# Kernel tuning notes

Hardware: AMD Instinct MI355X
Metric: run time of the kernel (lower is better)

Reference implementation:

```python
import jax, jax.numpy as jnp
import numpy as np

N = 30000   # fluid particles
E = 480000  # edges
F = 4       # fluidFeatures (in channels)
P = 8       # RBF basis size per dim (dims=[8], 1D)
LAYERS = [32, 64, 64, 2]


def hat_basis(x, n):
    # 'linear' RBF: hat functions on n evenly spaced centers in [-1, 1]
    centers = jnp.linspace(-1.0, 1.0, n, dtype=x.dtype)
    spacing = 2.0 / (n - 1)
    return jnp.maximum(0.0, 1.0 - jnp.abs(x[:, None] - centers[None, :]) / spacing)  # [E, n]


def rbf_conv(x, fi, fj, d, W, b, mask, n_nodes):
    # x: [N, Cin]; d: [E, 1] clamped; W: [P, Cin, Cout]; b: [Cout]
    phi = hat_basis(d[:, 0], W.shape[0])      # [E, P]
    xj = x[fj]                                 # gather source features [E, Cin]
    msg = jnp.zeros((xj.shape[0], W.shape[2]), dtype=x.dtype)
    for p in range(W.shape[0]):                # small fixed P=8 loop keeps memory O(E*Cout)
        msg = msg + phi[:, p, None] * (xj @ W[p])
    msg = jnp.where(mask[:, None], msg, 0.0)   # centerIgnore: drop self edges fi==fj
    out = jax.ops.segment_sum(msg, fi, num_segments=n_nodes)  # scatter-reduce to targets
    return out + b


def _xavier(key, shape_in, shape_out):
    lim = float(np.sqrt(6.0 / (shape_in + shape_out)))
    return jax.random.uniform(key, (shape_in, shape_out), jnp.float32, -lim, lim)


def setup_inputs() -> dict:
    key = jax.random.key(0)
    ks = jax.random.split(key, 16)
    fluidFeatures = jax.random.normal(ks[0], (N, F), jnp.float32)
    fi = jax.random.randint(ks[1], (E,), 0, N)
    fj = jax.random.randint(ks[2], (E,), 0, N)
    distances = jax.random.normal(ks[3], (E, 1), jnp.float32)
    # conv channels: 4->32, 64->64, 64->64, 64->2
    cio = [(F, 32), (2 * 32, 64), (64, 64), (64, 2)]
    inp = {"fluidFeatures": fluidFeatures, "fi": fi, "fj": fj, "distances": distances}
    for li, (ci, co) in enumerate(cio):
        inp[f"cW{li}"] = jax.random.normal(ks[4 + li], (P, ci, co), jnp.float32) * (1.0 / np.sqrt(P * ci))
        inp[f"cb{li}"] = jnp.zeros((co,), jnp.float32)
        inp[f"fW{li}"] = _xavier(ks[8 + li], ci, co)   # stored [in, out]
        inp[f"fb{li}"] = jnp.zeros((co,), jnp.float32)
    return inp


def reference(fluidFeatures, fi, fj, distances,
              cW0, cb0, fW0, fb0, cW1, cb1, fW1, fb1,
              cW2, cb2, fW2, fb2, cW3, cb3, fW3, fb3):
    n_nodes = fluidFeatures.shape[0]
    mask = fi != fj                     # centerIgnore (mask instead of filter: jit-safe)
    d = jnp.clip(distances, -1.0, 1.0)

    conv0 = rbf_conv(fluidFeatures, fi, fj, d, cW0, cb0, mask, n_nodes)  # [N, 32]
    lin0 = fluidFeatures @ fW0 + fb0                                      # [N, 32]
    ans = jnp.concatenate([lin0, conv0], axis=1)                          # [N, 64]

    # i = 1: features[0]=32 != features[1]=64 -> no residual
    ansc = jax.nn.relu(ans)
    ans = rbf_conv(ansc, fi, fj, d, cW1, cb1, mask, n_nodes) + (ansc @ fW1 + fb1)
    # i = 2: features[1]==features[2]==64 and shapes match -> residual
    ansc = jax.nn.relu(ans)
    ans = rbf_conv(ansc, fi, fj, d, cW2, cb2, mask, n_nodes) + (ansc @ fW2 + fb2) + ans
    # i = 3: 64 -> 2, no residual
    ansc = jax.nn.relu(ans)
    ans = rbf_conv(ansc, fi, fj, d, cW3, cb3, mask, n_nodes) + (ansc @ fW3 + fb3)

    return ans  # dim == 1 (dims=[8]) -> no /128
```

## Files before the change

kernel.cpp:

```cpp
#include <hip/hip_runtime.h>


#define CAP 48

typedef __attribute__((ext_vector_type(8))) short short8;
typedef __attribute__((ext_vector_type(4))) short short4v;
typedef __attribute__((ext_vector_type(4))) float f32x4;

__device__ __forceinline__ short bf16s(float f) {
  unsigned u = __float_as_uint(f);
  return (short)((u + 0x7FFF + ((u >> 16) & 1)) >> 16);
}
__device__ __forceinline__ float b2f(unsigned short s) {
  return __uint_as_float(((unsigned)s) << 16);
}
__device__ __forceinline__ unsigned pack2(float a, float b) {
  return (unsigned)(unsigned short)bf16s(a) | ((unsigned)(unsigned short)bf16s(b) << 16);
}

__global__ void fill_prep(const float* __restrict__ dist,
                          const int* __restrict__ fi, const int* __restrict__ fj,
                          int* __restrict__ cnt, int* __restrict__ jw, int nE,
                          const float* __restrict__ cW1, const float* __restrict__ fW1,
                          const float* __restrict__ cW2, const float* __restrict__ fW2,
                          short* __restrict__ wt1, short* __restrict__ wt2,
                          const float* __restrict__ X,
                          const float* __restrict__ cW0,
                          const float* __restrict__ fW0,
                          unsigned short* __restrict__ U0, int n,
                          int fillBlocks, int prepBlocks) {
  if ((int)blockIdx.x < fillBlocks) {
    int e = blockIdx.x * blockDim.x + threadIdx.x;
    if (e >= nE) return;
    int i = fi[e], j = fj[e];
    if (i == j) return;
    float d = fminf(1.0f, fmaxf(-1.0f, dist[e]));
    float u = (d + 1.0f) * 3.5f;
    int p = min((int)u, 6);
    float w0 = 1.0f - (u - (float)p);
    int wq = (int)(w0 * 16383.0f + 0.5f);
    int pos = atomicAdd(&cnt[i], 1);
    if (pos < CAP)
      jw[(size_t)i * CAP + pos] = j | (p << 15) | (wq << 18);
  } else if ((int)blockIdx.x < fillBlocks + prepBlocks) {
    int idx = ((int)blockIdx.x - fillBlocks) * blockDim.x + threadIdx.x;
    if (idx >= 2 * 576 * 64) return;
    int sel = idx / (576 * 64);
    int r = idx - sel * (576 * 64);
    int col = r >> 6, ch = r & 63;
    const float* cW = sel ? cW2 : cW1;
    const float* fW = sel ? fW2 : fW1;
    float v;
    if (col < 512) {
      int p = col >> 6, co = col & 63;
      v = cW[((size_t)p * 64 + ch) * 64 + co];
    } else {
      v = fW[(size_t)ch * 64 + (col - 512)];
    }
    (sel ? wt2 : wt1)[(size_t)col * 64 + ch] = bf16s(v);
  } else {
    int idx = ((int)blockIdx.x - fillBlocks - prepBlocks) * blockDim.x + threadIdx.x;
    if (idx >= n * 72) return;
    int i = idx / 72, g = idx - i * 72;
    float4 x = *(const float4*)(X + (size_t)i * 4);
    float xk[4] = {x.x, x.y, x.z, x.w};
    float s[4] = {0, 0, 0, 0};
    if (g < 64) {
      int p = g >> 3;
      int co = (g * 4) & 31;
      #pragma unroll
      for (int k = 0; k < 4; ++k) {
        const float* wr = cW0 + ((size_t)p * 4 + k) * 32 + co;
        #pragma unroll
        for (int c = 0; c < 4; ++c) s[c] = fmaf(xk[k], wr[c], s[c]);
      }
    } else {
      int co = (g - 64) * 4;
      #pragma unroll
      for (int k = 0; k < 4; ++k) {
        const float* wr = fW0 + (size_t)k * 32 + co;
        #pragma unroll
        for (int c = 0; c < 4; ++c) s[c] = fmaf(xk[k], wr[c], s[c]);
      }
    }
    uint2 pk = make_uint2(pack2(s[0], s[1]), pack2(s[2], s[3]));
    *(uint2*)(U0 + (size_t)i * 288 + g * 4) = pk;
  }
}

__global__ __launch_bounds__(1024) void layer0_gemm(
    const unsigned short* __restrict__ U0,
    const int* __restrict__ cnt, const int* __restrict__ jw,
    const float* __restrict__ cb0, const float* __restrict__ fb0,
    const short* __restrict__ WTul,
    unsigned short* __restrict__ UL, int n) {
  __shared__ __align__(16) unsigned short sXa[16 * 64];
  __shared__ __align__(16) short sUL[16 * 584];
  const int tid = threadIdx.x;
  const int w = tid >> 6;
  const int lane = tid & 63;
  const int grp = lane >> 5;
  const int gl = lane & 31;
  const int nodeBase = blockIdx.x * 16;
  const int i = nodeBase + w;
  const bool valid = (i < n);
  const int ic = valid ? i : 0;

  int rec = jw[(size_t)ic * CAP + (lane < CAP ? lane : 0)];
  const int m = valid ? min(cnt[ic], CAP) : 0;
  const int mc = m - 1;
  float accLo = 0.0f, accHi = 0.0f;
  for (int q0 = 0; q0 < m; q0 += 16) {
    unsigned raw[8];
    float ws[8];
    #pragma unroll
    for (int k = 0; k < 8; ++k) {
      int eA = q0 + 2 * k;
      int vA = __builtin_amdgcn_readlane(rec, min(eA, mc));
      int vB = __builtin_amdgcn_readlane(rec, min(eA + 1, mc));
      int v = grp ? vB : vA;
      int j = v & 0x7FFF;
      int p = (v >> 15) & 7;
      float w0 = (float)((unsigned)v >> 18) * (1.0f / 16383.0f);
      float wgt = (gl < 16) ? w0 : (1.0f - w0);
      ws[k] = (eA + grp < m) ? wgt : 0.0f;
      raw[k] = ((const unsigned*)(U0 + (size_t)j * 288 + p * 32))[gl];
    }
    #pragma unroll
    for (int k = 0; k < 8; ++k) {
      accLo = fmaf(ws[k], __uint_as_float(raw[k] << 16), accLo);
      accHi = fmaf(ws[k], __uint_as_float(raw[k] & 0xFFFF0000u), accHi);
    }
  }
  accLo += __shfl_xor(accLo, 16, 64);
  accHi += __shfl_xor(accHi, 16, 64);
  accLo += __shfl_xor(accLo, 32, 64);
  accHi += __shfl_xor(accHi, 32, 64);
  if (lane < 16) {
    const int l = lane;
    float c0v = fmaxf(accLo + cb0[2 * l], 0.0f);
    float c1v = fmaxf(accHi + cb0[2 * l + 1], 0.0f);
    unsigned lr = ((const unsigned*)(U0 + (size_t)ic * 288 + 256))[l];
    float l0 = fmaxf(__uint_as_float(lr << 16) + fb0[2 * l], 0.0f);
    float l1 = fmaxf(__uint_as_float(lr & 0xFFFF0000u) + fb0[2 * l + 1], 0.0f);
    unsigned* row = (unsigned*)(sXa + w * 64);
    row[l] = pack2(l0, l1);
    row[16 + l] = pack2(c0v, c1v);
  }
  __syncthreads();

  const int mrow = lane & 15;
  const int quad = lane >> 4;
  short8 b0 = *(const short8*)(sXa + mrow * 64 + quad * 8);
  short8 b1 = *(const short8*)(sXa + mrow * 64 + quad * 8 + 32);
  for (int t = w; t < 36; t += 16) {
    const short* aBase = WTul + (size_t)(t * 16 + mrow) * 64 + quad * 8;
    short8 a0 = *(const short8*)(aBase);
    short8 a1 = *(const short8*)(aBase + 32);
    f32x4 acc = {0, 0, 0, 0};
    acc = __builtin_amdgcn_mfma_f32_16x16x32_bf16(a0, b0, acc, 0, 0, 0);
    acc = __builtin_amdgcn_mfma_f32_16x16x32_bf16(a1, b1, acc, 0, 0, 0);
    short4v pk;
    #pragma unroll
    for (int reg = 0; reg < 4; ++reg) pk[reg] = bf16s(acc[reg]);
    *(short4v*)(sUL + mrow * 584 + t * 16 + quad * 4) = pk;
  }
  __syncthreads();
  const int r = tid >> 6;
  const int c0 = tid & 63;
  if (nodeBase + r < n) {
    unsigned short* dst = UL + (size_t)(nodeBase + r) * 576;
    #pragma unroll
    for (int chunk = c0; chunk < 72; chunk += 64)
      *(short8*)(dst + chunk * 8) = *(const short8*)(sUL + r * 584 + chunk * 8);
  }
}

__global__ __launch_bounds__(1024) void conv_gemm(
    const unsigned short* __restrict__ ULA,
    const int* __restrict__ cnt, const int* __restrict__ jw,
    const float* __restrict__ cb, const float* __restrict__ fb,
    const short* __restrict__ WTul2,
    float* __restrict__ outAns,
    unsigned short* __restrict__ ULB, int n) {
  __shared__ __align__(16) unsigned short sXa[16 * 64];
  __shared__ __align__(16) short sUL[16 * 584];
  const int tid = threadIdx.x;
  const int w = tid >> 6;
  const int lane = tid & 63;
  const int half = lane >> 5;
  const int pl = lane & 31;
  const int nodeBase = blockIdx.x * 16;
  const int i = nodeBase + w;
  const bool valid = (i < n);
  const int ic = valid ? i : 0;

  int rec = jw[(size_t)ic * CAP + (lane < CAP ? lane : 0)];
  const int m = valid ? min(cnt[ic], CAP) : 0;
  const int mc = m - 1;
  const unsigned Lraw = ((const unsigned*)(ULA + (size_t)ic * 576 + 512))[pl];
  float accLo = 0.0f, accHi = 0.0f;
  for (int q0 = 0; q0 < m; q0 += 16) {
    unsigned raw[16];
    float w0s[16];
    #pragma unroll
    for (int k = 0; k < 16; ++k) {
      int v = __builtin_amdgcn_readlane(rec, min(q0 + k, mc));
      int j = v & 0x7FFF;
      int p = (v >> 15) & 7;
      w0s[k] = (float)((unsigned)v >> 18) * (1.0f / 16383.0f);
      raw[k] = ((const unsigned*)(ULA + (size_t)j * 576 + p * 64))[lane];
    }
    #pragma unroll
    for (int k = 0; k < 16; ++k) {
      bool ok = (q0 + k < m);
      float wv = half ? (1.0f - w0s[k]) : w0s[k];
      wv = ok ? wv : 0.0f;
      accLo = fmaf(wv, __uint_as_float(raw[k] << 16), accLo);
      accHi = fmaf(wv, __uint_as_float(raw[k] & 0xFFFF0000u), accHi);
    }
  }
  accLo += __shfl_xor(accLo, 32, 64);
  accHi += __shfl_xor(accHi, 32, 64);
  if (half == 0) {
    unsigned* row = (unsigned*)(sXa + w * 64);
    if (valid) {
      const int c0i = 2 * pl, c1i = c0i + 1;
      float o0 = accLo + __uint_as_float(Lraw << 16) + cb[c0i] + fb[c0i];
      float o1 = accHi + __uint_as_float(Lraw & 0xFFFF0000u) + cb[c1i] + fb[c1i];
      *(float2*)(outAns + (size_t)i * 64 + c0i) = make_float2(o0, o1);
      row[pl] = pack2(fmaxf(o0, 0.0f), fmaxf(o1, 0.0f));
    } else {
      row[pl] = 0u;
    }
  }
  __syncthreads();

  const int mrow = lane & 15;
  const int quad = lane >> 4;
  short8 b0 = *(const short8*)(sXa + mrow * 64 + quad * 8);
  short8 b1 = *(const short8*)(sXa + mrow * 64 + quad * 8 + 32);
  for (int t = w; t < 36; t += 16) {
    const short* aBase = WTul2 + (size_t)(t * 16 + mrow) * 64 + quad * 8;
    short8 a0 = *(const short8*)(aBase);
    short8 a1 = *(const short8*)(aBase + 32);
    f32x4 acc = {0, 0, 0, 0};
    acc = __builtin_amdgcn_mfma_f32_16x16x32_bf16(a0, b0, acc, 0, 0, 0);
    acc = __builtin_amdgcn_mfma_f32_16x16x32_bf16(a1, b1, acc, 0, 0, 0);
    short4v pk;
    #pragma unroll
    for (int reg = 0; reg < 4; ++reg) pk[reg] = bf16s(acc[reg]);
    *(short4v*)(sUL + mrow * 584 + t * 16 + quad * 4) = pk;
  }
  __syncthreads();
  const int r = tid >> 6;
  const int c0 = tid & 63;
  if (nodeBase + r < n) {
    unsigned short* dst = ULB + (size_t)(nodeBase + r) * 576;
    #pragma unroll
    for (int chunk = c0; chunk < 72; chunk += 64)
      *(short8*)(dst + chunk * 8) = *(const short8*)(sUL + r * 584 + chunk * 8);
  }
}

__global__ __launch_bounds__(256) void conv2_kernel(
    const unsigned short* __restrict__ UL,
    const int* __restrict__ cnt, const int* __restrict__ jw,
    const float* __restrict__ cb, const float* __restrict__ fb,
    const float* __restrict__ resid,
    const float* __restrict__ cW3,
    float* __restrict__ T,
    unsigned short* __restrict__ outAnsc, int n) {
  const int lane = threadIdx.x & 63;
  const int half = lane >> 5;
  const int pl = lane & 31;
  const int i = (blockIdx.x * blockDim.x + threadIdx.x) >> 6;
  if (i >= n) return;
  int rec = jw[(size_t)i * CAP + (lane < CAP ? lane : 0)];
  const int m = min(cnt[i], CAP);
  const int mc = m - 1;
  const unsigned Lraw = ((const unsigned*)(UL + (size_t)i * 576 + 512))[pl];
  float2 rv = *(const float2*)(resid + (size_t)i * 64 + 2 * pl);
  float accLo = 0.0f, accHi = 0.0f;
  for (int q0 = 0; q0 < m; q0 += 16) {
    unsigned raw[16];
    float w0s[16];
    #pragma unroll
    for (int k = 0; k < 16; ++k) {
      int v = __builtin_amdgcn_readlane(rec, min(q0 + k, mc));
      int j = v & 0x7FFF;
      int p = (v >> 15) & 7;
      w0s[k] = (float)((unsigned)v >> 18) * (1.0f / 16383.0f);
      raw[k] = ((const unsigned*)(UL + (size_t)j * 576 + p * 64))[lane];
    }
    #pragma unroll
    for (int k = 0; k < 16; ++k) {
      bool ok = (q0 + k < m);
      float wv = half ? (1.0f - w0s[k]) : w0s[k];
      wv = ok ? wv : 0.0f;
      accLo = fmaf(wv, __uint_as_float(raw[k] << 16), accLo);
      accHi = fmaf(wv, __uint_as_float(raw[k] & 0xFFFF0000u), accHi);
    }
  }
  accLo += __shfl_xor(accLo, 32, 64);
  accHi += __shfl_xor(accHi, 32, 64);
  if (half == 0) {
    const int c0i = 2 * pl, c1i = c0i + 1;
    float o0 = accLo + __uint_as_float(Lraw << 16) + cb[c0i] + fb[c0i] + rv.x;
    float o1 = accHi + __uint_as_float(Lraw & 0xFFFF0000u) + cb[c1i] + fb[c1i] + rv.y;
    unsigned short xb0 = (unsigned short)bf16s(fmaxf(o0, 0.0f));
    unsigned short xb1 = (unsigned short)bf16s(fmaxf(o1, 0.0f));
    ((unsigned*)(outAnsc + (size_t)i * 64))[pl] = (unsigned)xb0 | ((unsigned)xb1 << 16);
    float x0 = b2f(xb0), x1 = b2f(xb1);
    float c[16];
    #pragma unroll
    for (int t = 0; t < 16; ++t) {
      const float* wrow = cW3 + ((size_t)(t >> 1) * 64) * 2 + (t & 1);
      c[t] = x0 * wrow[c0i * 2] + x1 * wrow[c1i * 2];
    }
    #pragma unroll
    for (int off = 16; off > 0; off >>= 1) {
      #pragma unroll
      for (int t = 0; t < 16; ++t) c[t] += __shfl_xor(c[t], off, 64);
    }
    if (pl == 0) {
      float* tr = T + (size_t)i * 16;
      #pragma unroll
      for (int t = 0; t < 16; ++t) tr[t] = c[t];
    }
  }
}

__global__ __launch_bounds__(256, 4) void layer3_kernel(
    const unsigned short* __restrict__ Xb,
    const float* __restrict__ T,
    const int* __restrict__ cnt, const int* __restrict__ jw,
    const float* __restrict__ cb3, const float* __restrict__ fb3,
    const float* __restrict__ fW3,
    float* __restrict__ out, int n) {
  const int lane = threadIdx.x & 63;
  const int i = (blockIdx.x * blockDim.x + threadIdx.x) >> 6;
  if (i >= n) return;
  const int m = min(cnt[i], CAP);
  float c0 = 0.0f, c1 = 0.0f;
  if (lane < m) {
    int v = jw[(size_t)i * CAP + lane];
    int j = min(v & 0x7FFF, n - 1);
    int p = (v >> 15) & 7;
    float w0 = (float)((unsigned)v >> 18) * (1.0f / 16383.0f);
    float w1 = 1.0f - w0;
    const float* tb = T + (size_t)j * 16 + p * 2;
    float2 ta = *(const float2*)(tb);
    float2 tc = *(const float2*)(tb + 2);
    c0 = w0 * ta.x + w1 * tc.x;
    c1 = w0 * ta.y + w1 * tc.y;
  }
  float xi = b2f(Xb[(size_t)i * 64 + lane]);
  float2 fw = *(const float2*)(fW3 + lane * 2);
  c0 = fmaf(xi, fw.x, c0);
  c1 = fmaf(xi, fw.y, c1);
  #pragma unroll
  for (int off = 32; off > 0; off >>= 1) {
    c0 += __shfl_xor(c0, off, 64);
    c1 += __shfl_xor(c1, off, 64);
  }
  if (lane == 0) {
    out[(size_t)i * 2 + 0] = c0 + cb3[0] + fb3[0];
    out[(size_t)i * 2 + 1] = c1 + cb3[1] + fb3[1];
  }
}

extern "C" void kernel_launch(void* const* d_in, const int* in_sizes, int n_in,
                              void* d_out, int out_size, void* d_ws, size_t ws_size,
                              hipStream_t stream) {
  const float* X    = (const float*)d_in[0];
  const int*   fi   = (const int*)d_in[1];
  const int*   fj   = (const int*)d_in[2];
  const float* dist = (const float*)d_in[3];
  const float* cW0 = (const float*)d_in[4];  const float* cb0 = (const float*)d_in[5];
  const float* fW0 = (const float*)d_in[6];  const float* fb0 = (const float*)d_in[7];
  const float* cW1 = (const float*)d_in[8];  const float* cb1 = (const float*)d_in[9];
  const float* fW1 = (const float*)d_in[10]; const float* fb1 = (const float*)d_in[11];
  const float* cW2 = (const float*)d_in[12]; const float* cb2 = (const float*)d_in[13];
  const float* fW2 = (const float*)d_in[14]; const float* fb2 = (const float*)d_in[15];
  const float* cW3 = (const float*)d_in[16]; const float* cb3 = (const float*)d_in[17];
  const float* fW3 = (const float*)d_in[18]; const float* fb3 = (const float*)d_in[19];
  float* out = (float*)d_out;

  const int n  = in_sizes[0] / 4;
  const int nE = in_sizes[1];

  unsigned short* ULA   = (unsigned short*)d_ws;
  unsigned short* ULB   = ULA + (size_t)n * 576;
  unsigned short* U0    = ULB;
  float*          ans1  = (float*)(ULB + (size_t)n * 576);
  unsigned short* ansc2 = (unsigned short*)(ans1 + (size_t)n * 64);
  float* T     = (float*)(ansc2 + (size_t)n * 64);
  short* wtul1 = (short*)(T + (size_t)n * 16);
  short* wtul2 = wtul1 + 576 * 64;
  int*   jw    = (int*)(wtul2 + 576 * 64);
  int*   cnt   = jw + (size_t)n * CAP;

  hipMemsetAsync(cnt, 0, (size_t)n * sizeof(int), stream);
  const int fillBlocks = (nE + 255) / 256;
  const int prepBlocks = (2 * 576 * 64 + 255) / 256;
  const int u0Blocks   = (n * 72 + 255) / 256;
  fill_prep<<<fillBlocks + prepBlocks + u0Blocks, 256, 0, stream>>>(
      dist, fi, fj, cnt, jw, nE, cW1, fW1, cW2, fW2, wtul1, wtul2,
      X, cW0, fW0, U0, n, fillBlocks, prepBlocks);

  layer0_gemm<<<(n + 15) / 16, 1024, 0, stream>>>(U0, cnt, jw, cb0, fb0,
                                                  wtul1, ULA, n);
  conv_gemm<<<(n + 15) / 16, 1024, 0, stream>>>(ULA, cnt, jw, cb1, fb1,
                                                wtul2, ans1, ULB, n);
  conv2_kernel<<<(n * 64 + 255) / 256, 256, 0, stream>>>(
      ULB, cnt, jw, cb2, fb2, ans1, cW3, T, ansc2, n);
  layer3_kernel<<<(n * 64 + 255) / 256, 256, 0, stream>>>(ansc2, T, cnt, jw,
                                                          cb3, fb3, fW3, out, n);
}
```

Measured before the change: 251.3 us.

## Issue two gather batches up front and unroll MFMA tail across all tiles

The edge-gather loops in the layer-0, conv, and conv2 kernels now issue the first two 16-edge batches of neighbour loads before any FMA, with sched_barrier separating loads from math, so more loads are in flight per wave. Edge weights are recomputed from the packed record at FMA time rather than held in registers. The MFMA projection tail is factored into a helper that loads all weight tiles for a wave (2 or 3) before issuing MFMAs, and launch bounds add a min-blocks hint of 8. This trades higher register pressure and some redundant readlanes for more memory-level parallelism, with a risk of spills or lower occupancy.

Result: faster. 246.3 us (-2.0%).

```diff
diff --git a/kernel.cpp b/kernel.cpp
--- a/kernel.cpp
+++ b/kernel.cpp
@@ -88,7 +88,51 @@
   }
 }
 
-__global__ __launch_bounds__(1024) void layer0_gemm(
+__device__ __forceinline__ void gemm_tail(const unsigned short* sXa, short* sUL,
+                                          const short* __restrict__ WT,
+                                          int w, int lane) {
+  const int mrow = lane & 15;
+  const int quad = lane >> 4;
+  short8 b0 = *(const short8*)(sXa + mrow * 64 + quad * 8);
+  short8 b1 = *(const short8*)(sXa + mrow * 64 + quad * 8 + 32);
+  const short* A0 = WT + (size_t)(w * 16 + mrow) * 64 + quad * 8;
+  const short* A1 = WT + (size_t)((w + 16) * 16 + mrow) * 64 + quad * 8;
+  short8 a00 = *(const short8*)(A0);
+  short8 a01 = *(const short8*)(A0 + 32);
+  short8 a10 = *(const short8*)(A1);
+  short8 a11 = *(const short8*)(A1 + 32);
+  const bool has3 = (w < 4);
+  short8 a20 = {0, 0, 0, 0, 0, 0, 0, 0};
+  short8 a21 = {0, 0, 0, 0, 0, 0, 0, 0};
+  if (has3) {
+    const short* A2 = WT + (size_t)((w + 32) * 16 + mrow) * 64 + quad * 8;
+    a20 = *(const short8*)(A2);
+    a21 = *(const short8*)(A2 + 32);
+  }
+  __builtin_amdgcn_sched_barrier(0);
+  f32x4 acc0 = {0, 0, 0, 0}, acc1 = {0, 0, 0, 0};
+  acc0 = __builtin_amdgcn_mfma_f32_16x16x32_bf16(a00, b0, acc0, 0, 0, 0);
+  acc0 = __builtin_amdgcn_mfma_f32_16x16x32_bf16(a01, b1, acc0, 0, 0, 0);
+  acc1 = __builtin_amdgcn_mfma_f32_16x16x32_bf16(a10, b0, acc1, 0, 0, 0);
+  acc1 = __builtin_amdgcn_mfma_f32_16x16x32_bf16(a11, b1, acc1, 0, 0, 0);
+  short4v pk;
+  #pragma unroll
+  for (int r = 0; r < 4; ++r) pk[r] = bf16s(acc0[r]);
+  *(short4v*)(sUL + mrow * 584 + w * 16 + quad * 4) = pk;
+  #pragma unroll
+  for (int r = 0; r < 4; ++r) pk[r] = bf16s(acc1[r]);
+  *(short4v*)(sUL + mrow * 584 + (w + 16) * 16 + quad * 4) = pk;
+  if (has3) {
+    f32x4 acc2 = {0, 0, 0, 0};
+    acc2 = __builtin_amdgcn_mfma_f32_16x16x32_bf16(a20, b0, acc2, 0, 0, 0);
+    acc2 = __builtin_amdgcn_mfma_f32_16x16x32_bf16(a21, b1, acc2, 0, 0, 0);
+    #pragma unroll
+    for (int r = 0; r < 4; ++r) pk[r] = bf16s(acc2[r]);
+    *(short4v*)(sUL + mrow * 584 + (w + 32) * 16 + quad * 4) = pk;
+  }
+}
+
+__global__ __launch_bounds__(1024, 8) void layer0_gemm(
     const unsigned short* __restrict__ U0,
     const int* __restrict__ cnt, const int* __restrict__ jw,
     const float* __restrict__ cb0, const float* __restrict__ fb0,
@@ -110,28 +154,45 @@
   const int m = valid ? min(cnt[ic], CAP) : 0;
   const int mc = m - 1;
   float accLo = 0.0f, accHi = 0.0f;
-  for (int q0 = 0; q0 < m; q0 += 16) {
-    unsigned raw[8];
-    float ws[8];
-    #pragma unroll
-    for (int k = 0; k < 8; ++k) {
-      int eA = q0 + 2 * k;
-      int vA = __builtin_amdgcn_readlane(rec, min(eA, mc));
-      int vB = __builtin_amdgcn_readlane(rec, min(eA + 1, mc));
-      int v = grp ? vB : vA;
-      int j = v & 0x7FFF;
-      int p = (v >> 15) & 7;
-      float w0 = (float)((unsigned)v >> 18) * (1.0f / 16383.0f);
-      float wgt = (gl < 16) ? w0 : (1.0f - w0);
-      ws[k] = (eA + grp < m) ? wgt : 0.0f;
-      raw[k] = ((const unsigned*)(U0 + (size_t)j * 288 + p * 32))[gl];
-    }
-    #pragma unroll
-    for (int k = 0; k < 8; ++k) {
-      accLo = fmaf(ws[k], __uint_as_float(raw[k] << 16), accLo);
-      accHi = fmaf(ws[k], __uint_as_float(raw[k] & 0xFFFF0000u), accHi);
-    }
-  }
+  const unsigned* __restrict__ u0W = (const unsigned*)U0;
+  unsigned rA[8], rB[8];
+  float wA[8], wB[8];
+#define L0_LOAD(R, WS, Q0)                                                  \
+  _Pragma("unroll")                                                         \
+  for (int k = 0; k < 8; ++k) {                                             \
+    int eA = (Q0) + 2 * k;                                                  \
+    int vA = __builtin_amdgcn_readlane(rec, min(eA, mc));                   \
+    int vB = __builtin_amdgcn_readlane(rec, min(eA + 1, mc));               \
+    int v = grp ? vB : vA;                                                  \
+    int j = v & 0x7FFF;                                                     \
+    int p = (v >> 15) & 7;                                                  \
+    float w0 = (float)((unsigned)v >> 18) * (1.0f / 16383.0f);              \
+    float wgt = (gl < 16) ? w0 : (1.0f - w0);                               \
+    WS[k] = (eA + grp < m) ? wgt : 0.0f;                                    \
+    R[k] = u0W[(size_t)j * 144 + p * 16 + gl];                              \
+  }
+#define L0_FMA(R, WS)                                                       \
+  _Pragma("unroll")                                                         \
+  for (int k = 0; k < 8; ++k) {                                             \
+    accLo = fmaf(WS[k], __uint_as_float(R[k] << 16), accLo);                \
+    accHi = fmaf(WS[k], __uint_as_float(R[k] & 0xFFFF0000u), accHi);        \
+  }
+  if (m > 0) {
+    L0_LOAD(rA, wA, 0);
+    L0_LOAD(rB, wB, 16);
+    __builtin_amdgcn_sched_barrier(0);
+    L0_FMA(rA, wA);
+    if (m > 16) {
+      L0_FMA(rB, wB);
+      for (int q0 = 32; q0 < m; q0 += 16) {
+        L0_LOAD(rA, wA, q0);
+        __builtin_amdgcn_sched_barrier(0);
+        L0_FMA(rA, wA);
+      }
+    }
+  }
+#undef L0_LOAD
+#undef L0_FMA
   accLo += __shfl_xor(accLo, 16, 64);
   accHi += __shfl_xor(accHi, 16, 64);
   accLo += __shfl_xor(accLo, 32, 64);
@@ -149,22 +210,7 @@
   }
   __syncthreads();
 
-  const int mrow = lane & 15;
-  const int quad = lane >> 4;
-  short8 b0 = *(const short8*)(sXa + mrow * 64 + quad * 8);
-  short8 b1 = *(const short8*)(sXa + mrow * 64 + quad * 8 + 32);
-  for (int t = w; t < 36; t += 16) {
-    const short* aBase = WTul + (size_t)(t * 16 + mrow) * 64 + quad * 8;
-    short8 a0 = *(const short8*)(aBase);
-    short8 a1 = *(const short8*)(aBase + 32);
-    f32x4 acc = {0, 0, 0, 0};
-    acc = __builtin_amdgcn_mfma_f32_16x16x32_bf16(a0, b0, acc, 0, 0, 0);
-    acc = __builtin_amdgcn_mfma_f32_16x16x32_bf16(a1, b1, acc, 0, 0, 0);
-    short4v pk;
-    #pragma unroll
-    for (int reg = 0; reg < 4; ++reg) pk[reg] = bf16s(acc[reg]);
-    *(short4v*)(sUL + mrow * 584 + t * 16 + quad * 4) = pk;
-  }
+  gemm_tail(sXa, sUL, WTul, w, lane);
   __syncthreads();
   const int r = tid >> 6;
   const int c0 = tid & 63;
@@ -176,7 +222,7 @@
   }
 }
 
-__global__ __launch_bounds__(1024) void conv_gemm(
+__global__ __launch_bounds__(1024, 8) void conv_gemm(
     const unsigned short* __restrict__ ULA,
     const int* __restrict__ cnt, const int* __restrict__ jw,
     const float* __restrict__ cb, const float* __restrict__ fb,
@@ -200,26 +246,42 @@
   const int mc = m - 1;
   const unsigned Lraw = ((const unsigned*)(ULA + (size_t)ic * 576 + 512))[pl];
   float accLo = 0.0f, accHi = 0.0f;
-  for (int q0 = 0; q0 < m; q0 += 16) {
-    unsigned raw[16];
-    float w0s[16];
-    #pragma unroll
-    for (int k = 0; k < 16; ++k) {
-      int v = __builtin_amdgcn_readlane(rec, min(q0 + k, mc));
-      int j = v & 0x7FFF;
-      int p = (v >> 15) & 7;
-      w0s[k] = (float)((unsigned)v >> 18) * (1.0f / 16383.0f);
-      raw[k] = ((const unsigned*)(ULA + (size_t)j * 576 + p * 64))[lane];
-    }
-    #pragma unroll
-    for (int k = 0; k < 16; ++k) {
-      bool ok = (q0 + k < m);
-      float wv = half ? (1.0f - w0s[k]) : w0s[k];
-      wv = ok ? wv : 0.0f;
-      accLo = fmaf(wv, __uint_as_float(raw[k] << 16), accLo);
-      accHi = fmaf(wv, __uint_as_float(raw[k] & 0xFFFF0000u), accHi);
-    }
-  }
+  const unsigned* __restrict__ ulaW = (const unsigned*)ULA;
+  unsigned rA[16], rB[16];
+#define C1_LOAD(R, Q0)                                                      \
+  _Pragma("unroll")                                                         \
+  for (int k = 0; k < 16; ++k) {                                            \
+    int v = __builtin_amdgcn_readlane(rec, min((Q0) + k, mc));              \
+    int j = v & 0x7FFF;                                                     \
+    int p = (v >> 15) & 7;                                                  \
+    R[k] = ulaW[(size_t)j * 288 + p * 32 + lane];                           \
+  }
+#define C1_FMA(R, Q0)                                                       \
+  _Pragma("unroll")                                                         \
+  for (int k = 0; k < 16; ++k) {                                            \
+    int v = __builtin_amdgcn_readlane(rec, min((Q0) + k, mc));              \
+    float w0 = (float)((unsigned)v >> 18) * (1.0f / 16383.0f);              \
+    float wv = half ? (1.0f - w0) : w0;                                     \
+    wv = ((Q0) + k < m) ? wv : 0.0f;                                        \
+    accLo = fmaf(wv, __uint_as_float(R[k] << 16), accLo);                   \
+    accHi = fmaf(wv, __uint_as_float(R[k] & 0xFFFF0000u), accHi);           \
+  }
+  if (m > 0) {
+    C1_LOAD(rA, 0);
+    C1_LOAD(rB, 16);
+    __builtin_amdgcn_sched_barrier(0);
+    C1_FMA(rA, 0);
+    if (m > 16) {
+      C1_FMA(rB, 16);
+      for (int q0 = 32; q0 < m; q0 += 16) {
+        C1_LOAD(rA, q0);
+        __builtin_amdgcn_sched_barrier(0);
+        C1_FMA(rA, q0);
+      }
+    }
+  }
+#undef C1_LOAD
+#undef C1_FMA
   accLo += __shfl_xor(accLo, 32, 64);
   accHi += __shfl_xor(accHi, 32, 64);
   if (half == 0) {
@@ -236,22 +298,7 @@
   }
   __syncthreads();
 
-  const int mrow = lane & 15;
-  const int quad = lane >> 4;
-  short8 b0 = *(const short8*)(sXa + mrow * 64 + quad * 8);
-  short8 b1 = *(const short8*)(sXa + mrow * 64 + quad * 8 + 32);
-  for (int t = w; t < 36; t += 16) {
-    const short* aBase = WTul2 + (size_t)(t * 16 + mrow) * 64 + quad * 8;
-    short8 a0 = *(const short8*)(aBase);
-    short8 a1 = *(const short8*)(aBase + 32);
-    f32x4 acc = {0, 0, 0, 0};
-    acc = __builtin_amdgcn_mfma_f32_16x16x32_bf16(a0, b0, acc, 0, 0, 0);
-    acc = __builtin_amdgcn_mfma_f32_16x16x32_bf16(a1, b1, acc, 0, 0, 0);
-    short4v pk;
-    #pragma unroll
-    for (int reg = 0; reg < 4; ++reg) pk[reg] = bf16s(acc[reg]);
-    *(short4v*)(sUL + mrow * 584 + t * 16 + quad * 4) = pk;
-  }
+  gemm_tail(sXa, sUL, WTul2, w, lane);
   __syncthreads();
   const int r = tid >> 6;
   const int c0 = tid & 63;
@@ -263,7 +310,7 @@
   }
 }
 
-__global__ __launch_bounds__(256) void conv2_kernel(
+__global__ __launch_bounds__(256, 8) void conv2_kernel(
     const unsigned short* __restrict__ UL,
     const int* __restrict__ cnt, const int* __restrict__ jw,
     const float* __restrict__ cb, const float* __restrict__ fb,
@@ -282,26 +329,42 @@
   const unsigned Lraw = ((const unsigned*)(UL + (size_t)i * 576 + 512))[pl];
   float2 rv = *(const float2*)(resid + (size_t)i * 64 + 2 * pl);
   float accLo = 0.0f, accHi = 0.0f;
-  for (int q0 = 0; q0 < m; q0 += 16) {
-    unsigned raw[16];
-    float w0s[16];
-    #pragma unroll
-    for (int k = 0; k < 16; ++k) {
-      int v = __builtin_amdgcn_readlane(rec, min(q0 + k, mc));
-      int j = v & 0x7FFF;
-      int p = (v >> 15) & 7;
-      w0s[k] = (float)((unsigned)v >> 18) * (1.0f / 16383.0f);
-      raw[k] = ((const unsigned*)(UL + (size_t)j * 576 + p * 64))[lane];
-    }
-    #pragma unroll
-    for (int k = 0; k < 16; ++k) {
-      bool ok = (q0 + k < m);
-      float wv = half ? (1.0f - w0s[k]) : w0s[k];
-      wv = ok ? wv : 0.0f;
-      accLo = fmaf(wv, __uint_as_float(raw[k] << 16), accLo);
-      accHi = fmaf(wv, __uint_as_float(raw[k] & 0xFFFF0000u), accHi);
-    }
-  }
+  const unsigned* __restrict__ ulW = (const unsigned*)UL;
+  unsigned rA[16], rB[16];
+#define C2_LOAD(R, Q0)                                                      \
+  _Pragma("unroll")                                                         \
+  for (int k = 0; k < 16; ++k) {                                            \
+    int v = __builtin_amdgcn_readlane(rec, min((Q0) + k, mc));              \
+    int j = v & 0x7FFF;                                                     \
+    int p = (v >> 15) & 7;                                                  \
+    R[k] = ulW[(size_t)j * 288 + p * 32 + lane];                            \
+  }
+#define C2_FMA(R, Q0)                                                       \
+  _Pragma("unroll")                                                         \
+  for (int k = 0; k < 16; ++k) {                                            \
+    int v = __builtin_amdgcn_readlane(rec, min((Q0) + k, mc));              \
+    float w0 = (float)((unsigned)v >> 18) * (1.0f / 16383.0f);              \
+    float wv = half ? (1.0f - w0) : w0;                                     \
+    wv = ((Q0) + k < m) ? wv : 0.0f;                                        \
+    accLo = fmaf(wv, __uint_as_float(R[k] << 16), accLo);                   \
+    accHi = fmaf(wv, __uint_as_float(R[k] & 0xFFFF0000u), accHi);           \
+  }
+  if (m > 0) {
+    C2_LOAD(rA, 0);
+    C2_LOAD(rB, 16);
+    __builtin_amdgcn_sched_barrier(0);
+    C2_FMA(rA, 0);
+    if (m > 16) {
+      C2_FMA(rB, 16);
+      for (int q0 = 32; q0 < m; q0 += 16) {
+        C2_LOAD(rA, q0);
+        __builtin_amdgcn_sched_barrier(0);
+        C2_FMA(rA, q0);
+      }
+    }
+  }
+#undef C2_LOAD
+#undef C2_FMA
   accLo += __shfl_xor(accLo, 32, 64);
   accHi += __shfl_xor(accHi, 32, 64);
   if (half == 0) {
```

## Re-encode edge records with precomputed offsets and gather via scalar loads into LDS

Applied to the files above, without the earlier changes.

Edge records now store a precomputed row offset (j*9+p) plus a 12-bit weight and a valid flag. Zeroing the whole record table lets padded slots contribute zero weight without per-edge bounds checks. The aggregation kernels read a node's records with scalar s_load_dwordx4 and gather neighbour rows straight into LDS with global_load_lds, replacing per-lane readlane decoding and register gathers. GEMM blocks shrink from 16 to 8 nodes (512 threads) to raise occupancy, and T rows are padded to 18 floats so the offset encoding indexes it directly. The cost is inline asm with manual waitcnts, lower weight precision, and a larger memset.

Result: slower. 268.0 us (+6.6%).

```diff
diff --git a/kernel.cpp b/kernel.cpp
--- a/kernel.cpp
+++ b/kernel.cpp
@@ -6,6 +6,7 @@
 typedef __attribute__((ext_vector_type(8))) short short8;
 typedef __attribute__((ext_vector_type(4))) short short4v;
 typedef __attribute__((ext_vector_type(4))) float f32x4;
+typedef int v4i __attribute__((ext_vector_type(4)));
 
 __device__ __forceinline__ short bf16s(float f) {
   unsigned u = __float_as_uint(f);
@@ -17,6 +18,61 @@
 __device__ __forceinline__ unsigned pack2(float a, float b) {
   return (unsigned)(unsigned short)bf16s(a) | ((unsigned)(unsigned short)bf16s(b) << 16);
 }
+__device__ __forceinline__ float dec_w0(int v) {
+  return __uint_as_float(0x3F800000u | (((unsigned)v & 0xFFFu) << 11)) - 1.0f;
+}
+__device__ __forceinline__ float dec_sf(int v) {
+  return (float)(((unsigned)v >> 12) & 1u);
+}
+__device__ __forceinline__ unsigned long long rfl64(unsigned long long x) {
+  unsigned lo = __builtin_amdgcn_readfirstlane((unsigned)x);
+  unsigned hi = __builtin_amdgcn_readfirstlane((unsigned)(x >> 32));
+  return ((unsigned long long)hi << 32) | (unsigned long long)lo;
+}
+__device__ __forceinline__ void gload_lds4(const void* g, void* l) {
+  __builtin_amdgcn_global_load_lds(
+      (const __attribute__((address_space(1))) void*)g,
+      (__attribute__((address_space(3))) void*)l, 4, 0, 0);
+}
+
+#define WAIT_VM0 asm volatile("s_waitcnt vmcnt(0)" ::: "memory")
+#define WAIT_LGKM0 asm volatile("s_waitcnt lgkmcnt(0)" ::: "memory")
+
+#define LOAD_RECS32Q(JROW, CPTR, MRAW)                                      \
+  v4i q0, q1, q2, q3, q4, q5, q6, q7;                                       \
+  int MRAW;                                                                 \
+  asm volatile("s_load_dwordx4 %0, %9, 0x0\n\t"                             \
+               "s_load_dwordx4 %1, %9, 0x10\n\t"                            \
+               "s_load_dwordx4 %2, %9, 0x20\n\t"                            \
+               "s_load_dwordx4 %3, %9, 0x30\n\t"                            \
+               "s_load_dwordx4 %4, %9, 0x40\n\t"                            \
+               "s_load_dwordx4 %5, %9, 0x50\n\t"                            \
+               "s_load_dwordx4 %6, %9, 0x60\n\t"                            \
+               "s_load_dwordx4 %7, %9, 0x70\n\t"                            \
+               "s_load_dword %8, %10, 0x0\n\t"                              \
+               "s_waitcnt lgkmcnt(0)"                                       \
+               : "=&s"(q0), "=&s"(q1), "=&s"(q2), "=&s"(q3), "=&s"(q4),     \
+                 "=&s"(q5), "=&s"(q6), "=&s"(q7), "=&s"(MRAW)               \
+               : "s"(JROW), "s"(CPTR)                                       \
+               : "memory")
+
+#define LOAD_RECS16TQ(JROW)                                                 \
+  v4i qt0, qt1, qt2, qt3;                                                   \
+  asm volatile("s_load_dwordx4 %0, %4, 0x80\n\t"                            \
+               "s_load_dwordx4 %1, %4, 0x90\n\t"                            \
+               "s_load_dwordx4 %2, %4, 0xA0\n\t"                            \
+               "s_load_dwordx4 %3, %4, 0xB0\n\t"                            \
+               "s_waitcnt lgkmcnt(0)"                                       \
+               : "=&s"(qt0), "=&s"(qt1), "=&s"(qt2), "=&s"(qt3)             \
+               : "s"(JROW)                                                  \
+               : "memory")
+
+#define RECK(K) ((K) < 4 ? q0[(K) & 3] : (K) < 8 ? q1[(K) & 3] :            \
+                 (K) < 12 ? q2[(K) & 3] : (K) < 16 ? q3[(K) & 3] :          \
+                 (K) < 20 ? q4[(K) & 3] : (K) < 24 ? q5[(K) & 3] :          \
+                 (K) < 28 ? q6[(K) & 3] : q7[(K) & 3])
+#define RECT(K) ((K) < 4 ? qt0[(K) & 3] : (K) < 8 ? qt1[(K) & 3] :          \
+                 (K) < 12 ? qt2[(K) & 3] : qt3[(K) & 3])
 
 __global__ void fill_prep(const float* __restrict__ dist,
                           const int* __restrict__ fi, const int* __restrict__ fj,
@@ -38,10 +94,11 @@
     float u = (d + 1.0f) * 3.5f;
     int p = min((int)u, 6);
     float w0 = 1.0f - (u - (float)p);
-    int wq = (int)(w0 * 16383.0f + 0.5f);
+    int wq = min((int)(w0 * 4096.0f + 0.5f), 4095);
+    unsigned off = (unsigned)(j * 9 + p);
     int pos = atomicAdd(&cnt[i], 1);
     if (pos < CAP)
-      jw[(size_t)i * CAP + pos] = j | (p << 15) | (wq << 18);
+      jw[(size_t)i * CAP + pos] = (int)((off << 13) | 0x1000u | (unsigned)wq);
   } else if ((int)blockIdx.x < fillBlocks + prepBlocks) {
     int idx = ((int)blockIdx.x - fillBlocks) * blockDim.x + threadIdx.x;
     if (idx >= 2 * 576 * 64) return;
@@ -88,50 +145,91 @@
   }
 }
 
-__global__ __launch_bounds__(1024) void layer0_gemm(
+__device__ __forceinline__ void gemm_tail8(const unsigned short* sXa, short* sUL,
+                                           const short* __restrict__ WT,
+                                           int w, int lane) {
+  const int mrow = lane & 15;
+  const int quad = lane >> 4;
+  short8 b0 = *(const short8*)(sXa + mrow * 64 + quad * 8);
+  short8 b1 = *(const short8*)(sXa + mrow * 64 + quad * 8 + 32);
+  for (int t = w; t < 36; t += 8) {
+    const short* A = WT + (size_t)(t * 16 + mrow) * 64 + quad * 8;
+    short8 a0 = *(const short8*)(A);
+    short8 a1 = *(const short8*)(A + 32);
+    f32x4 acc = {0, 0, 0, 0};
+    acc = __builtin_amdgcn_mfma_f32_16x16x32_bf16(a0, b0, acc, 0, 0, 0);
+    acc = __builtin_amdgcn_mfma_f32_16x16x32_bf16(a1, b1, acc, 0, 0, 0);
+    short4v pk;
+    #pragma unroll
+    for (int r = 0; r < 4; ++r) pk[r] = bf16s(acc[r]);
+    *(short4v*)(sUL + mrow * 584 + t * 16 + quad * 4) = pk;
+  }
+}
+
+__global__ __launch_bounds__(512, 8) void layer0_gemm(
     const unsigned short* __restrict__ U0,
     const int* __restrict__ cnt, const int* __restrict__ jw,
     const float* __restrict__ cb0, const float* __restrict__ fb0,
     const short* __restrict__ WTul,
     unsigned short* __restrict__ UL, int n) {
+  __shared__ __align__(16) char smem[8 * 4096];
   __shared__ __align__(16) unsigned short sXa[16 * 64];
-  __shared__ __align__(16) short sUL[16 * 584];
   const int tid = threadIdx.x;
   const int w = tid >> 6;
   const int lane = tid & 63;
   const int grp = lane >> 5;
   const int gl = lane & 31;
-  const int nodeBase = blockIdx.x * 16;
+  const unsigned gl4 = (unsigned)gl * 4u;
+  const int nodeBase = blockIdx.x * 8;
   const int i = nodeBase + w;
   const bool valid = (i < n);
   const int ic = valid ? i : 0;
-
-  int rec = jw[(size_t)ic * CAP + (lane < CAP ? lane : 0)];
-  const int m = valid ? min(cnt[ic], CAP) : 0;
-  const int mc = m - 1;
+  if (tid < 256) ((unsigned*)sXa)[256 + tid] = 0u;
+  const int* jrow = (const int*)rfl64((unsigned long long)(jw + (size_t)ic * CAP));
+  const int* cptr = (const int*)rfl64((unsigned long long)(cnt + ic));
+  LOAD_RECS32Q(jrow, cptr, mraw);
+  const int m = valid ? min(mraw, CAP) : 0;
+  char* ldsW = smem + w * 4096;
+  unsigned* ldsWu = (unsigned*)ldsW;
+  const char* u0B = (const char*)U0;
   float accLo = 0.0f, accHi = 0.0f;
-  for (int q0 = 0; q0 < m; q0 += 16) {
-    unsigned raw[8];
-    float ws[8];
-    #pragma unroll
-    for (int k = 0; k < 8; ++k) {
-      int eA = q0 + 2 * k;
-      int vA = __builtin_amdgcn_readlane(rec, min(eA, mc));
-      int vB = __builtin_amdgcn_readlane(rec, min(eA + 1, mc));
-      int v = grp ? vB : vA;
-      int j = v & 0x7FFF;
-      int p = (v >> 15) & 7;
-      float w0 = (float)((unsigned)v >> 18) * (1.0f / 16383.0f);
-      float wgt = (gl < 16) ? w0 : (1.0f - w0);
-      ws[k] = (eA + grp < m) ? wgt : 0.0f;
-      raw[k] = ((const unsigned*)(U0 + (size_t)j * 288 + p * 32))[gl];
-    }
-    #pragma unroll
-    for (int k = 0; k < 8; ++k) {
-      accLo = fmaf(ws[k], __uint_as_float(raw[k] << 16), accLo);
-      accHi = fmaf(ws[k], __uint_as_float(raw[k] & 0xFFFF0000u), accHi);
-    }
-  }
+#define L0_ISSUE(K, RE)                                                     \
+  { int v_ = grp ? RE(2 * (K) + 1) : RE(2 * (K));                           \
+    unsigned soff_ = (((unsigned)v_) >> 7) & 0xFFFFFFC0u;                   \
+    gload_lds4(u0B + soff_ + gl4, ldsW + (K) * 256); }
+#define L0_CONS(K, RE)                                                      \
+  { int v_ = grp ? RE(2 * (K) + 1) : RE(2 * (K));                           \
+    float w0_ = dec_w0(v_);                                                 \
+    float wgt_ = (gl < 16) ? w0_ : (dec_sf(v_) - w0_);                      \
+    unsigned rd_ = ldsWu[(K) * 64 + lane];                                  \
+    accLo = fmaf(wgt_, __uint_as_float(rd_ << 16), accLo);                  \
+    accHi = fmaf(wgt_, __uint_as_float(rd_ & 0xFFFF0000u), accHi); }
+  if (m > 0) {
+    if (m <= 16) {
+      #pragma unroll
+      for (int k = 0; k < 8; ++k) L0_ISSUE(k, RECK);
+      WAIT_VM0;
+      #pragma unroll
+      for (int k = 0; k < 8; ++k) L0_CONS(k, RECK);
+    } else {
+      #pragma unroll
+      for (int k = 0; k < 16; ++k) L0_ISSUE(k, RECK);
+      WAIT_VM0;
+      #pragma unroll
+      for (int k = 0; k < 16; ++k) L0_CONS(k, RECK);
+      if (m > 32) {
+        LOAD_RECS16TQ(jrow);
+        WAIT_LGKM0;
+        #pragma unroll
+        for (int k = 0; k < 8; ++k) L0_ISSUE(k, RECT);
+        WAIT_VM0;
+        #pragma unroll
+        for (int k = 0; k < 8; ++k) L0_CONS(k, RECT);
+      }
+    }
+  }
+#undef L0_ISSUE
+#undef L0_CONS
   accLo += __shfl_xor(accLo, 16, 64);
   accHi += __shfl_xor(accHi, 16, 64);
   accLo += __shfl_xor(accLo, 32, 64);
@@ -149,77 +247,84 @@
   }
   __syncthreads();
 
-  const int mrow = lane & 15;
-  const int quad = lane >> 4;
-  short8 b0 = *(const short8*)(sXa + mrow * 64 + quad * 8);
-  short8 b1 = *(const short8*)(sXa + mrow * 64 + quad * 8 + 32);
-  for (int t = w; t < 36; t += 16) {
-    const short* aBase = WTul + (size_t)(t * 16 + mrow) * 64 + quad * 8;
-    short8 a0 = *(const short8*)(aBase);
-    short8 a1 = *(const short8*)(aBase + 32);
-    f32x4 acc = {0, 0, 0, 0};
-    acc = __builtin_amdgcn_mfma_f32_16x16x32_bf16(a0, b0, acc, 0, 0, 0);
-    acc = __builtin_amdgcn_mfma_f32_16x16x32_bf16(a1, b1, acc, 0, 0, 0);
-    short4v pk;
-    #pragma unroll
-    for (int reg = 0; reg < 4; ++reg) pk[reg] = bf16s(acc[reg]);
-    *(short4v*)(sUL + mrow * 584 + t * 16 + quad * 4) = pk;
-  }
+  gemm_tail8(sXa, (short*)smem, WTul, w, lane);
   __syncthreads();
-  const int r = tid >> 6;
+  const int r2 = tid >> 6;
   const int c0 = tid & 63;
-  if (nodeBase + r < n) {
-    unsigned short* dst = UL + (size_t)(nodeBase + r) * 576;
+  if (nodeBase + r2 < n) {
+    const short* sUL = (const short*)smem;
+    unsigned short* dst = UL + (size_t)(nodeBase + r2) * 576;
     #pragma unroll
     for (int chunk = c0; chunk < 72; chunk += 64)
-      *(short8*)(dst + chunk * 8) = *(const short8*)(sUL + r * 584 + chunk * 8);
-  }
-}
-
-__global__ __launch_bounds__(1024) void conv_gemm(
+      *(short8*)(dst + chunk * 8) = *(const short8*)(sUL + r2 * 584 + chunk * 8);
+  }
+}
+
+__global__ __launch_bounds__(512, 8) void conv_gemm(
     const unsigned short* __restrict__ ULA,
     const int* __restrict__ cnt, const int* __restrict__ jw,
     const float* __restrict__ cb, const float* __restrict__ fb,
     const short* __restrict__ WTul2,
     float* __restrict__ outAns,
     unsigned short* __restrict__ ULB, int n) {
+  __shared__ __align__(16) char smem[8 * 4096];
   __shared__ __align__(16) unsigned short sXa[16 * 64];
-  __shared__ __align__(16) short sUL[16 * 584];
   const int tid = threadIdx.x;
   const int w = tid >> 6;
   const int lane = tid & 63;
   const int half = lane >> 5;
   const int pl = lane & 31;
-  const int nodeBase = blockIdx.x * 16;
+  const unsigned lane4 = (unsigned)lane * 4u;
+  const int nodeBase = blockIdx.x * 8;
   const int i = nodeBase + w;
   const bool valid = (i < n);
   const int ic = valid ? i : 0;
-
-  int rec = jw[(size_t)ic * CAP + (lane < CAP ? lane : 0)];
-  const int m = valid ? min(cnt[ic], CAP) : 0;
-  const int mc = m - 1;
+  if (tid < 256) ((unsigned*)sXa)[256 + tid] = 0u;
+  const int* jrow = (const int*)rfl64((unsigned long long)(jw + (size_t)ic * CAP));
+  const int* cptr = (const int*)rfl64((unsigned long long)(cnt + ic));
+  LOAD_RECS32Q(jrow, cptr, mraw);
+  const int m = valid ? min(mraw, CAP) : 0;
   const unsigned Lraw = ((const unsigned*)(ULA + (size_t)ic * 576 + 512))[pl];
+  char* ldsW = smem + w * 4096;
+  unsigned* ldsWu = (unsigned*)ldsW;
+  const char* ulB = (const char*)ULA;
   float accLo = 0.0f, accHi = 0.0f;
-  for (int q0 = 0; q0 < m; q0 += 16) {
-    unsigned raw[16];
-    float w0s[16];
-    #pragma unroll
-    for (int k = 0; k < 16; ++k) {
-      int v = __builtin_amdgcn_readlane(rec, min(q0 + k, mc));
-      int j = v & 0x7FFF;
-      int p = (v >> 15) & 7;
-      w0s[k] = (float)((unsigned)v >> 18) * (1.0f / 16383.0f);
-      raw[k] = ((const unsigned*)(ULA + (size_t)j * 576 + p * 64))[lane];
-    }
-    #pragma unroll
-    for (int k = 0; k < 16; ++k) {
-      bool ok = (q0 + k < m);
-      float wv = half ? (1.0f - w0s[k]) : w0s[k];
-      wv = ok ? wv : 0.0f;
-      accLo = fmaf(wv, __uint_as_float(raw[k] << 16), accLo);
-      accHi = fmaf(wv, __uint_as_float(raw[k] & 0xFFFF0000u), accHi);
-    }
-  }
+#define CV_ISSUE(K, RE)                                                     \
+  { unsigned soff_ = (((unsigned)RE(K)) >> 6) & 0xFFFFFF80u;                \
+    gload_lds4(ulB + soff_ + lane4, ldsW + ((K) & 15) * 256); }
+#define CV_CONS(K, RE)                                                      \
+  { int v_ = RE(K);                                                         \
+    float w0_ = dec_w0(v_);                                                 \
+    float wv_ = half ? (dec_sf(v_) - w0_) : w0_;                            \
+    unsigned rd_ = ldsWu[((K) & 15) * 64 + lane];                           \
+    accLo = fmaf(wv_, __uint_as_float(rd_ << 16), accLo);                   \
+    accHi = fmaf(wv_, __uint_as_float(rd_ & 0xFFFF0000u), accHi); }
+  if (m > 0) {
+    #pragma unroll
+    for (int k = 0; k < 16; ++k) CV_ISSUE(k, RECK);
+    WAIT_VM0;
+    #pragma unroll
+    for (int k = 0; k < 16; ++k) CV_CONS(k, RECK);
+    if (m > 16) {
+      WAIT_LGKM0;
+      #pragma unroll
+      for (int k = 16; k < 32; ++k) CV_ISSUE(k, RECK);
+      WAIT_VM0;
+      #pragma unroll
+      for (int k = 16; k < 32; ++k) CV_CONS(k, RECK);
+      if (m > 32) {
+        LOAD_RECS16TQ(jrow);
+        WAIT_LGKM0;
+        #pragma unroll
+        for (int k = 0; k < 16; ++k) CV_ISSUE(k, RECT);
+        WAIT_VM0;
+        #pragma unroll
+        for (int k = 0; k < 16; ++k) CV_CONS(k, RECT);
+      }
+    }
+  }
+#undef CV_ISSUE
+#undef CV_CONS
   accLo += __shfl_xor(accLo, 32, 64);
   accHi += __shfl_xor(accHi, 32, 64);
   if (half == 0) {
@@ -236,34 +341,20 @@
   }
   __syncthreads();
 
-  const int mrow = lane & 15;
-  const int quad = lane >> 4;
-  short8 b0 = *(const short8*)(sXa + mrow * 64 + quad * 8);
-  short8 b1 = *(const short8*)(sXa + mrow * 64 + quad * 8 + 32);
-  for (int t = w; t < 36; t += 16) {
-    const short* aBase = WTul2 + (size_t)(t * 16 + mrow) * 64 + quad * 8;
-    short8 a0 = *(const short8*)(aBase);
-    short8 a1 = *(const short8*)(aBase + 32);
-    f32x4 acc = {0, 0, 0, 0};
-    acc = __builtin_amdgcn_mfma_f32_16x16x32_bf16(a0, b0, acc, 0, 0, 0);
-    acc = __builtin_amdgcn_mfma_f32_16x16x32_bf16(a1, b1, acc, 0, 0, 0);
-    short4v pk;
-    #pragma unroll
-    for (int reg = 0; reg < 4; ++reg) pk[reg] = bf16s(acc[reg]);
-    *(short4v*)(sUL + mrow * 584 + t * 16 + quad * 4) = pk;
-  }
+  gemm_tail8(sXa, (short*)smem, WTul2, w, lane);
   __syncthreads();
-  const int r = tid >> 6;
+  const int r2 = tid >> 6;
   const int c0 = tid & 63;
-  if (nodeBase + r < n) {
-    unsigned short* dst = ULB + (size_t)(nodeBase + r) * 576;
+  if (nodeBase + r2 < n) {
+    const short* sUL = (const short*)smem;
+    unsigned short* dst = ULB + (size_t)(nodeBase + r2) * 576;
     #pragma unroll
     for (int chunk = c0; chunk < 72; chunk += 64)
-      *(short8*)(dst + chunk * 8) = *(const short8*)(sUL + r * 584 + chunk * 8);
-  }
-}
-
-__global__ __launch_bounds__(256) void conv2_kernel(
+      *(short8*)(dst + chunk * 8) = *(const short8*)(sUL + r2 * 584 + chunk * 8);
+  }
+}
+
+__global__ __launch_bounds__(256, 8) void conv2_kernel(
     const unsigned short* __restrict__ UL,
     const int* __restrict__ cnt, const int* __restrict__ jw,
     const float* __restrict__ cb, const float* __restrict__ fb,
@@ -271,37 +362,60 @@
     const float* __restrict__ cW3,
     float* __restrict__ T,
     unsigned short* __restrict__ outAnsc, int n) {
+  __shared__ __align__(16) char smem2[4 * 4096];
   const int lane = threadIdx.x & 63;
   const int half = lane >> 5;
   const int pl = lane & 31;
+  const unsigned lane4 = (unsigned)lane * 4u;
+  const int w4 = threadIdx.x >> 6;
   const int i = (blockIdx.x * blockDim.x + threadIdx.x) >> 6;
   if (i >= n) return;
-  int rec = jw[(size_t)i * CAP + (lane < CAP ? lane : 0)];
-  const int m = min(cnt[i], CAP);
-  const int mc = m - 1;
+  const int* jrow = (const int*)rfl64((unsigned long long)(jw + (size_t)i * CAP));
+  const int* cptr = (const int*)rfl64((unsigned long long)(cnt + i));
+  LOAD_RECS32Q(jrow, cptr, mraw);
+  const int m = min(mraw, CAP);
   const unsigned Lraw = ((const unsigned*)(UL + (size_t)i * 576 + 512))[pl];
   float2 rv = *(const float2*)(resid + (size_t)i * 64 + 2 * pl);
+  char* ldsW = smem2 + w4 * 4096;
+  unsigned* ldsWu = (unsigned*)ldsW;
+  const char* ulB = (const char*)UL;
   float accLo = 0.0f, accHi = 0.0f;
-  for (int q0 = 0; q0 < m; q0 += 16) {
-    unsigned raw[16];
-    float w0s[16];
-    #pragma unroll
-    for (int k = 0; k < 16; ++k) {
-      int v = __builtin_amdgcn_readlane(rec, min(q0 + k, mc));
-      int j = v & 0x7FFF;
-      int p = (v >> 15) & 7;
-      w0s[k] = (float)((unsigned)v >> 18) * (1.0f / 16383.0f);
-      raw[k] = ((const unsigned*)(UL + (size_t)j * 576 + p * 64))[lane];
-    }
-    #pragma unroll
-    for (int k = 0; k < 16; ++k) {
-      bool ok = (q0 + k < m);
-      float wv = half ? (1.0f - w0s[k]) : w0s[k];
-      wv = ok ? wv : 0.0f;
-      accLo = fmaf(wv, __uint_as_float(raw[k] << 16), accLo);
-      accHi = fmaf(wv, __uint_as_float(raw[k] & 0xFFFF0000u), accHi);
-    }
-  }
+#define CV_ISSUE(K, RE)                                                     \
+  { unsigned soff_ = (((unsigned)RE(K)) >> 6) & 0xFFFFFF80u;                \
+    gload_lds4(ulB + soff_ + lane4, ldsW + ((K) & 15) * 256); }
+#define CV_CONS(K, RE)                                                      \
+  { int v_ = RE(K);                                                         \
+    float w0_ = dec_w0(v_);                                                 \
+    float wv_ = half ? (dec_sf(v_) - w0_) : w0_;                            \
+    unsigned rd_ = ldsWu[((K) & 15) * 64 + lane];                           \
+    accLo = fmaf(wv_, __uint_as_float(rd_ << 16), accLo);                   \
+    accHi = fmaf(wv_, __uint_as_float(rd_ & 0xFFFF0000u), accHi); }
+  if (m > 0) {
+    #pragma unroll
+    for (int k = 0; k < 16; ++k) CV_ISSUE(k, RECK);
+    WAIT_VM0;
+    #pragma unroll
+    for (int k = 0; k < 16; ++k) CV_CONS(k, RECK);
+    if (m > 16) {
+      WAIT_LGKM0;
+      #pragma unroll
+      for (int k = 16; k < 32; ++k) CV_ISSUE(k, RECK);
+      WAIT_VM0;
+      #pragma unroll
+      for (int k = 16; k < 32; ++k) CV_CONS(k, RECK);
+      if (m > 32) {
+        LOAD_RECS16TQ(jrow);
+        WAIT_LGKM0;
+        #pragma unroll
+        for (int k = 0; k < 16; ++k) CV_ISSUE(k, RECT);
+        WAIT_VM0;
+        #pragma unroll
+        for (int k = 0; k < 16; ++k) CV_CONS(k, RECT);
+      }
+    }
+  }
+#undef CV_ISSUE
+#undef CV_CONS
   accLo += __shfl_xor(accLo, 32, 64);
   accHi += __shfl_xor(accHi, 32, 64);
   if (half == 0) {
@@ -324,7 +438,7 @@
       for (int t = 0; t < 16; ++t) c[t] += __shfl_xor(c[t], off, 64);
     }
     if (pl == 0) {
-      float* tr = T + (size_t)i * 16;
+      float* tr = T + (size_t)i * 18;
       #pragma unroll
       for (int t = 0; t < 16; ++t) tr[t] = c[t];
     }
@@ -345,11 +459,10 @@
   float c0 = 0.0f, c1 = 0.0f;
   if (lane < m) {
     int v = jw[(size_t)i * CAP + lane];
-    int j = min(v & 0x7FFF, n - 1);
-    int p = (v >> 15) & 7;
-    float w0 = (float)((unsigned)v >> 18) * (1.0f / 16383.0f);
+    unsigned off = (unsigned)v >> 13;
+    float w0 = dec_w0(v);
     float w1 = 1.0f - w0;
-    const float* tb = T + (size_t)j * 16 + p * 2;
+    const float* tb = T + (size_t)off * 2;
     float2 ta = *(const float2*)(tb);
     float2 tc = *(const float2*)(tb + 2);
     c0 = w0 * ta.x + w1 * tc.x;
@@ -396,12 +509,12 @@
   float*          ans1  = (float*)(ULB + (size_t)n * 576);
   unsigned short* ansc2 = (unsigned short*)(ans1 + (size_t)n * 64);
   float* T     = (float*)(ansc2 + (size_t)n * 64);
-  short* wtul1 = (short*)(T + (size_t)n * 16);
+  short* wtul1 = (short*)(T + (size_t)n * 18);
   short* wtul2 = wtul1 + 576 * 64;
   int*   jw    = (int*)(wtul2 + 576 * 64);
   int*   cnt   = jw + (size_t)n * CAP;
 
-  hipMemsetAsync(cnt, 0, (size_t)n * sizeof(int), stream);
+  hipMemsetAsync(jw, 0, ((size_t)n * CAP + n) * sizeof(int), stream);
   const int fillBlocks = (nE + 255) / 256;
   const int prepBlocks = (2 * 576 * 64 + 255) / 256;
   const int u0Blocks   = (n * 72 + 255) / 256;
@@ -409,10 +522,10 @@
       dist, fi, fj, cnt, jw, nE, cW1, fW1, cW2, fW2, wtul1, wtul2,
       X, cW0, fW0, U0, n, fillBlocks, prepBlocks);
 
-  layer0_gemm<<<(n + 15) / 16, 1024, 0, stream>>>(U0, cnt, jw, cb0, fb0,
-                                                  wtul1, ULA, n);
-  conv_gemm<<<(n + 15) / 16, 1024, 0, stream>>>(ULA, cnt, jw, cb1, fb1,
-                                                wtul2, ans1, ULB, n);
+  layer0_gemm<<<(n + 7) / 8, 512, 0, stream>>>(U0, cnt, jw, cb0, fb0,
+                                               wtul1, ULA, n);
+  conv_gemm<<<(n + 7) / 8, 512, 0, stream>>>(ULA, cnt, jw, cb1, fb1,
+                                             wtul2, ans1, ULB, n);
   conv2_kernel<<<(n * 64 + 255) / 256, 256, 0, stream>>>(
       ULB, cnt, jw, cb2, fb2, ans1, cW3, T, ansc2, n);
   layer3_kernel<<<(n * 64 + 255) / 256, 256, 0, stream>>>(ansc2, T, cnt, jw,
```
